# Kernel tuning notes

Measured on AMD Instinct MI355X. Metric: run time of the kernel, lower is better.

The kernel has to match this reference:

```python
import jax, jax.numpy as jnp
import numpy as np

N = 100000
E = 1600000
IN_DIM, H1, H2, C = 256, 128, 128, 32


def setup_inputs() -> dict:
    key = jax.random.key(0)
    ks = jax.random.split(key, 8)
    X = jax.random.normal(ks[0], (N, IN_DIM), dtype=jnp.float32)
    edge_index = jax.random.randint(ks[1], (2, E), 0, N, dtype=jnp.int64)
    def glorot(k, shape):
        fan_in, fan_out = shape[0], shape[1]
        lim = (6.0 / (fan_in + fan_out)) ** 0.5
        return jax.random.uniform(k, shape, jnp.float32, -lim, lim)
    W1 = glorot(ks[2], (IN_DIM, H1))
    b1 = jnp.zeros((H1,), jnp.float32)
    W2 = glorot(ks[3], (H1, H2))
    b2 = jnp.zeros((H2,), jnp.float32)
    Wc = glorot(ks[4], (H2, C))
    bc = jnp.zeros((C,), jnp.float32)
    return {"X": X, "edge_index": edge_index, "W1": W1, "b1": b1,
            "W2": W2, "b2": b2, "Wc": Wc, "bc": bc}


def gcn_conv(x, src, dst, dinv, W, b, n):
    # PyG GCNConv: transform, then sym-normalized scatter-add with self-loops
    x = x @ W  # [N, out]
    norm = dinv[src] * dinv[dst]  # [E+N]
    msgs = x[src] * norm[:, None]  # [E+N, out] gather along edges
    out = jax.ops.segment_sum(msgs, dst, num_segments=n)
    return out + b


def reference(X, edge_index, W1, b1, W2, b2, Wc, bc):
    n = X.shape[0]
    loop = jnp.arange(n, dtype=edge_index.dtype)
    src = jnp.concatenate([edge_index[0], loop])
    dst = jnp.concatenate([edge_index[1], loop])
    # degree (with self-loops) at destination nodes
    deg = jax.ops.segment_sum(jnp.ones_like(dst, jnp.float32), dst, num_segments=n)
    dinv = jnp.where(deg > 0, jax.lax.rsqrt(deg), 0.0)
    h = jax.nn.relu(gcn_conv(X, src, dst, dinv, W1, b1, n))
    h = jax.nn.relu(gcn_conv(h, src, dst, dinv, W2, b2, n))
    logits = h @ Wc + bc
    return logits
```

## Files before the change

kernel.cpp:

```cpp
#include <hip/hip_runtime.h>
#include <hip/hip_bf16.h>
#include <hip/hip_fp16.h>

#define IN_DIM 256
#define HDIM 128
#define CDIM 32
#define NSUB 512
#define PCHUNK 4096

typedef __attribute__((ext_vector_type(8))) unsigned short u16x8;
typedef __attribute__((ext_vector_type(8))) _Float16 f16x8;
typedef __attribute__((ext_vector_type(4))) float f32x4;
typedef __attribute__((ext_vector_type(4))) int int4v;

__device__ __forceinline__ int swz4(int r) { return (r & 3) ^ ((r >> 2) & 3); }


__global__ void zero512_kernel(int* __restrict__ p) {
    p[blockIdx.x * 256 + threadIdx.x] = 0;
}

__global__ __launch_bounds__(256) void hist512_kernel(const int* __restrict__ dst,
                                                      int* __restrict__ cnt512, int e, int nsr) {
    __shared__ int h[NSUB];
    for (int j = threadIdx.x; j < NSUB; j += 256) h[j] = 0;
    __syncthreads();
    const int stride = gridDim.x * 256;
    for (int i = blockIdx.x * 256 + threadIdx.x; i < e; i += stride) {
        int d = __builtin_nontemporal_load(&dst[i]);
        atomicAdd(&h[(unsigned)d / (unsigned)nsr], 1);
    }
    __syncthreads();
    for (int j = threadIdx.x; j < NSUB; j += 256)
        if (h[j]) atomicAdd(&cnt512[j], h[j]);
}

__global__ __launch_bounds__(256) void scan512_kernel(const int* __restrict__ cnt512,
                                                      int* __restrict__ rp512,
                                                      int* __restrict__ rcur512, int e) {
    __shared__ int sd[256];
    int t = threadIdx.x;
    int v0 = cnt512[2 * t], v1 = cnt512[2 * t + 1];
    sd[t] = v0 + v1;
    __syncthreads();
    for (int off = 1; off < 256; off <<= 1) {
        int x = (t >= off) ? sd[t - off] : 0;
        __syncthreads();
        sd[t] += x;
        __syncthreads();
    }
    int excl = sd[t] - (v0 + v1);
    rp512[2 * t] = excl;          rcur512[2 * t] = excl;
    rp512[2 * t + 1] = excl + v0; rcur512[2 * t + 1] = excl + v0;
    if (t == 255) rp512[512] = e;
}

__global__ __launch_bounds__(256) void part512_kernel(
        const int* __restrict__ src, const int* __restrict__ dst,
        int* __restrict__ rcur512, long long* __restrict__ parts, int e, int nsr) {
    __shared__ long long staged[PCHUNK];
    __shared__ int hist[NSUB], lbase[NSUB], gbase[NSUB], lcur[NSUB];
    __shared__ int sd[256];
    const int t = threadIdx.x;
    const int nch = (e + PCHUNK - 1) / PCHUNK;
    for (int c = blockIdx.x; c < nch; c += gridDim.x) {
        const int b0 = c * PCHUNK;
        const int cnt = (b0 + PCHUNK <= e) ? PCHUNK : (e - b0);
        int s[16], d[16], bn[16];
        hist[2 * t] = 0; hist[2 * t + 1] = 0;
        __syncthreads();
        if (cnt == PCHUNK) {
#pragma unroll
            for (int q = 0; q < 4; ++q) {
                int u = q * 256 + t;
                int4v sv = __builtin_nontemporal_load((const int4v*)(src + b0) + u);
                int4v dv = __builtin_nontemporal_load((const int4v*)(dst + b0) + u);
                s[4 * q] = sv.x; s[4 * q + 1] = sv.y; s[4 * q + 2] = sv.z; s[4 * q + 3] = sv.w;
                d[4 * q] = dv.x; d[4 * q + 1] = dv.y; d[4 * q + 2] = dv.z; d[4 * q + 3] = dv.w;
            }
#pragma unroll
            for (int j = 0; j < 16; ++j) {
                bn[j] = (int)((unsigned)d[j] / (unsigned)nsr);
                atomicAdd(&hist[bn[j]], 1);
            }
        } else {
#pragma unroll
            for (int j = 0; j < 16; ++j) {
                int u = (j / 4) * 1024 + t * 4 + (j & 3);
                int i = b0 + u;
                if (u < cnt) {
                    s[j] = src[i]; d[j] = dst[i];
                    bn[j] = (int)((unsigned)d[j] / (unsigned)nsr);
                    atomicAdd(&hist[bn[j]], 1);
                } else bn[j] = -1;
            }
        }
        __syncthreads();
        int h0 = hist[2 * t], h1 = hist[2 * t + 1];
        sd[t] = h0 + h1;
        __syncthreads();
        for (int off = 1; off < 256; off <<= 1) {
            int x = (t >= off) ? sd[t - off] : 0;
            __syncthreads();
            sd[t] += x;
            __syncthreads();
        }
        int excl = sd[t] - (h0 + h1);
        lbase[2 * t] = excl;          lcur[2 * t] = excl;
        lbase[2 * t + 1] = excl + h0; lcur[2 * t + 1] = excl + h0;
        gbase[2 * t]     = h0 ? atomicAdd(&rcur512[2 * t], h0) : 0;
        gbase[2 * t + 1] = h1 ? atomicAdd(&rcur512[2 * t + 1], h1) : 0;
        __syncthreads();
#pragma unroll
        for (int j = 0; j < 16; ++j) {
            if (bn[j] >= 0) {
                int pos = atomicAdd(&lcur[bn[j]], 1);
                staged[pos] = ((long long)(unsigned)d[j] << 32) | (unsigned)s[j];
            }
        }
        __syncthreads();
        for (int i = t; i < cnt; i += 256) {
            long long v = staged[i];
            int b = (int)((unsigned)(int)(v >> 32) / (unsigned)nsr);
            parts[gbase[b] + (i - lbase[b])] = v;
        }
        __syncthreads();
    }
}

__global__ __launch_bounds__(256) void sortplace_kernel(
        const long long* __restrict__ parts, const int* __restrict__ rp512,
        int* __restrict__ row_ptr, int* __restrict__ csr_src, float* __restrict__ dinv,
        int n, int nsr) {
    __shared__ int hist[256], sd[256], cur[256];
    const int b = blockIdx.x;
    const int d0 = b * nsr;
    if (d0 > n) return;
    const int i0 = rp512[b], iE = rp512[b + 1];
    const int t = threadIdx.x;
    hist[t] = 0;
    __syncthreads();
    for (int i = i0 + t; i < iE; i += 256) {
        int d = (int)(parts[i] >> 32);
        atomicAdd(&hist[d - d0], 1);
    }
    __syncthreads();
    int v = hist[t];
    sd[t] = v;
    __syncthreads();
    for (int off = 1; off < 256; off <<= 1) {
        int x = (t >= off) ? sd[t - off] : 0;
        __syncthreads();
        sd[t] += x;
        __syncthreads();
    }
    int excl = sd[t] - v;
    int node = d0 + t;
    if (t <= nsr && node <= n) row_ptr[node] = i0 + excl;
    if (t < nsr && node < n) dinv[node] = rsqrtf((float)(v + 1));
    cur[t] = i0 + excl;
    __syncthreads();
    for (int i = i0 + t; i < iE; i += 256) {
        long long vv = parts[i];
        int d = (int)(vv >> 32);
        int pos = atomicAdd(&cur[d - d0], 1);
        csr_src[pos] = (int)(vv & 0xffffffffLL);
    }
}


__global__ void wconv_all_kernel(const float* __restrict__ W1, const float* __restrict__ W2,
                                 const float* __restrict__ Wc,
                                 unsigned short* __restrict__ w1t, unsigned short* __restrict__ w2t,
                                 unsigned short* __restrict__ wct) {
    int i = blockIdx.x * 256 + threadIdx.x;
    const int s1 = IN_DIM * HDIM;
    const int s2 = s1 + HDIM * HDIM;
    const int s3 = s2 + HDIM * CDIM;
    if (i < s1) {
        int k = i / HDIM, n2 = i % HDIM;
        w1t[n2 * IN_DIM + k] = __half_as_ushort(__float2half_rn(W1[i]));
    } else if (i < s2) {
        int j = i - s1; int k = j / HDIM, n2 = j % HDIM;
        w2t[n2 * HDIM + k] = __half_as_ushort(__float2half_rn(W2[j]));
    } else if (i < s3) {
        int j = i - s2; int k = j / CDIM, n2 = j % CDIM;
        wct[n2 * HDIM + k] = __half_as_ushort(__float2half_rn(Wc[j]));
    }
}


template<int BN, bool AF16, bool BIAS, bool OUTH>
__global__ __launch_bounds__(256) void gemm_f16_kernel(
        const void* __restrict__ Ap, const unsigned short* __restrict__ Wt,
        const float* __restrict__ bias, void* __restrict__ C, int M, int K) {
    constexpr int FM = 4;
    constexpr int FN = BN / 2 / 16;
    constexpr int BU = (BN * 4 + 255) / 256;
    __shared__ __align__(16) unsigned short As[2][128 * 32];
    __shared__ __align__(16) unsigned short Bs[2][BN * 32];

    const int t = threadIdx.x;
    const int rowBase = blockIdx.x * 128;
    const int l = t & 63, w = t >> 6;
    const int wr = w >> 1, wc = w & 1;
    const int lrow = l & 15, g = l >> 4;
    const int NK = K >> 5;

    f32x4 acc[FM][FN];
#pragma unroll
    for (int i = 0; i < FM; ++i)
#pragma unroll
        for (int j = 0; j < FN; ++j) acc[i][j] = f32x4{0.f, 0.f, 0.f, 0.f};

    u16x8 aS[2];
    float4 af[2][2];
    u16x8 bS[BU];

    auto LOADA = [&](int k0) {
#pragma unroll
        for (int i = 0; i < 2; ++i) {
            int u = t + 256 * i;
            int r = u >> 2, c = u & 3;
            int gr = rowBase + r; if (gr > M - 1) gr = M - 1;
            if (AF16) {
                aS[i] = ((const u16x8*)((const unsigned short*)Ap + (size_t)gr * K + k0))[c];
            } else {
                const float4* ar = (const float4*)((const float*)Ap + (size_t)gr * K + k0);
                af[i][0] = ar[c * 2];
                af[i][1] = ar[c * 2 + 1];
            }
        }
    };
    auto WRITEA = [&](int buf) {
#pragma unroll
        for (int i = 0; i < 2; ++i) {
            int u = t + 256 * i;
            int r = u >> 2, c = u & 3;
            int d = r * 4 + (c ^ swz4(r));
            if (AF16) {
                ((u16x8*)As[buf])[d] = aS[i];
            } else {
                f16x8 h;
                h[0] = (_Float16)af[i][0].x; h[1] = (_Float16)af[i][0].y;
                h[2] = (_Float16)af[i][0].z; h[3] = (_Float16)af[i][0].w;
                h[4] = (_Float16)af[i][1].x; h[5] = (_Float16)af[i][1].y;
                h[6] = (_Float16)af[i][1].z; h[7] = (_Float16)af[i][1].w;
                ((f16x8*)As[buf])[d] = h;
            }
        }
    };
    auto LOADB = [&](int k0) {
#pragma unroll
        for (int i = 0; i < BU; ++i) {
            int u = t + 256 * i;
            if (u < BN * 4) {
                int nn = u >> 2, c = u & 3;
                bS[i] = ((const u16x8*)(Wt + (size_t)nn * K + k0))[c];
            }
        }
    };
    auto WRITEB = [&](int buf) {
#pragma unroll
        for (int i = 0; i < BU; ++i) {
            int u = t + 256 * i;
            if (u < BN * 4) {
                int nn = u >> 2, c = u & 3;
                ((u16x8*)Bs[buf])[nn * 4 + (c ^ swz4(nn))] = bS[i];
            }
        }
    };

    LOADA(0); LOADB(0);
    WRITEA(0); WRITEB(0);
    __syncthreads();

    for (int k = 0; k < NK; ++k) {
        int cur = k & 1;
        bool more = (k + 1 < NK);
        if (more) { LOADA((k + 1) << 5); LOADB((k + 1) << 5); }

        f16x8 a[FM], b[FN];
#pragma unroll
        for (int fm = 0; fm < FM; ++fm) {
            int r = wr * 64 + fm * 16 + lrow;
            a[fm] = ((const f16x8*)As[cur])[r * 4 + (g ^ swz4(r))];
        }
#pragma unroll
        for (int fn = 0; fn < FN; ++fn) {
            int nn = wc * (FN * 16) + fn * 16 + lrow;
            b[fn] = ((const f16x8*)Bs[cur])[nn * 4 + (g ^ swz4(nn))];
        }
#pragma unroll
        for (int fm = 0; fm < FM; ++fm)
#pragma unroll
            for (int fn = 0; fn < FN; ++fn)
                acc[fm][fn] = __builtin_amdgcn_mfma_f32_16x16x32_f16(a[fm], b[fn], acc[fm][fn], 0, 0, 0);

        if (more) { WRITEA(cur ^ 1); WRITEB(cur ^ 1); }
        __syncthreads();
    }

#pragma unroll
    for (int fm = 0; fm < FM; ++fm)
#pragma unroll
        for (int fn = 0; fn < FN; ++fn) {
            int col = wc * (FN * 16) + fn * 16 + lrow;
#pragma unroll
            for (int r = 0; r < 4; ++r) {
                int row = rowBase + wr * 64 + fm * 16 + g * 4 + r;
                if (row < M) {
                    float v = acc[fm][fn][r];
                    if (BIAS) v += bias[col];
                    if (OUTH) {
                        __builtin_nontemporal_store(
                            __half_as_ushort(__float2half_rn(v)),
                            (unsigned short*)C + (size_t)row * BN + col);
                    } else {
                        ((float*)C)[(size_t)row * BN + col] = v;
                    }
                }
            }
        }
}


__global__ __launch_bounds__(256) void gather_kernel(
        const __half* __restrict__ x, const int* __restrict__ row_ptr,
        const int* __restrict__ csr_src, const float* __restrict__ dinv,
        const float* __restrict__ bias, __half* __restrict__ out, int n) {
    int node = __builtin_amdgcn_readfirstlane(blockIdx.x * 4 + (threadIdx.x >> 6));
    if (node >= n) return;
    int lane = threadIdx.x & 63;
    const __half2* xv = (const __half2*)x;
    float dd = dinv[node];
    float2 self = __half22float2(xv[(size_t)node * 64 + lane]);
    float accx = dd * self.x, accy = dd * self.y;
    int p = row_ptr[node], end = row_ptr[node + 1];
    for (; p + 7 < end; p += 8) {
        int s[8]; float w[8]; float2 v[8];
#pragma unroll
        for (int j = 0; j < 8; ++j) s[j] = csr_src[p + j];
#pragma unroll
        for (int j = 0; j < 8; ++j) w[j] = dinv[s[j]];
#pragma unroll
        for (int j = 0; j < 8; ++j) v[j] = __half22float2(xv[(size_t)s[j] * 64 + lane]);
#pragma unroll
        for (int j = 0; j < 8; ++j) { accx += w[j] * v[j].x; accy += w[j] * v[j].y; }
    }
    for (; p + 3 < end; p += 4) {
        int s0 = csr_src[p], s1 = csr_src[p + 1], s2 = csr_src[p + 2], s3 = csr_src[p + 3];
        float w0 = dinv[s0], w1 = dinv[s1], w2 = dinv[s2], w3 = dinv[s3];
        float2 v0 = __half22float2(xv[(size_t)s0 * 64 + lane]);
        float2 v1 = __half22float2(xv[(size_t)s1 * 64 + lane]);
        float2 v2 = __half22float2(xv[(size_t)s2 * 64 + lane]);
        float2 v3 = __half22float2(xv[(size_t)s3 * 64 + lane]);
        accx += w0 * v0.x + w1 * v1.x + w2 * v2.x + w3 * v3.x;
        accy += w0 * v0.y + w1 * v1.y + w2 * v2.y + w3 * v3.y;
    }
    for (; p < end; ++p) {
        int s0 = csr_src[p];
        float w0 = dinv[s0];
        float2 v0 = __half22float2(xv[(size_t)s0 * 64 + lane]);
        accx += w0 * v0.x;
        accy += w0 * v0.y;
    }
    float2 bb = ((const float2*)bias)[lane];
    float2 r;
    r.x = fmaxf(accx * dd + bb.x, 0.f);
    r.y = fmaxf(accy * dd + bb.y, 0.f);
    __half2 hv = __float22half2_rn(r);
    __builtin_nontemporal_store(*(unsigned int*)&hv,
                                (unsigned int*)((__half2*)out + (size_t)node * 64 + lane));
}


__global__ __launch_bounds__(256) void gather_cls_kernel(
        const __half* __restrict__ x, const int* __restrict__ row_ptr,
        const int* __restrict__ csr_src, const float* __restrict__ dinv,
        const float* __restrict__ b2, const unsigned short* __restrict__ wct,
        const float* __restrict__ bc, float* __restrict__ out, int n) {
    __shared__ __align__(16) __half h_lds[16][136];
    const int w = threadIdx.x >> 6;
    const int lane = threadIdx.x & 63;
    const int node0 = blockIdx.x * 16;
    const __half2* xv = (const __half2*)x;
    const float2 bb = ((const float2*)b2)[lane];

#pragma unroll
    for (int j = 0; j < 4; ++j) {
        int row = w * 4 + j;
        int node = __builtin_amdgcn_readfirstlane(node0 + row);
        float2 rv = make_float2(0.f, 0.f);
        if (node < n) {
            float dd = dinv[node];
            float2 self = __half22float2(xv[(size_t)node * 64 + lane]);
            float accx = dd * self.x, accy = dd * self.y;
            int p = row_ptr[node], end = row_ptr[node + 1];
            for (; p + 7 < end; p += 8) {
                int s[8]; float wt[8]; float2 v[8];
#pragma unroll
                for (int q = 0; q < 8; ++q) s[q] = csr_src[p + q];
#pragma unroll
                for (int q = 0; q < 8; ++q) wt[q] = dinv[s[q]];
#pragma unroll
                for (int q = 0; q < 8; ++q) v[q] = __half22float2(xv[(size_t)s[q] * 64 + lane]);
#pragma unroll
                for (int q = 0; q < 8; ++q) { accx += wt[q] * v[q].x; accy += wt[q] * v[q].y; }
            }
            for (; p + 3 < end; p += 4) {
                int s0 = csr_src[p], s1 = csr_src[p + 1], s2 = csr_src[p + 2], s3 = csr_src[p + 3];
                float w0 = dinv[s0], w1 = dinv[s1], w2 = dinv[s2], w3 = dinv[s3];
                float2 v0 = __half22float2(xv[(size_t)s0 * 64 + lane]);
                float2 v1 = __half22float2(xv[(size_t)s1 * 64 + lane]);
                float2 v2 = __half22float2(xv[(size_t)s2 * 64 + lane]);
                float2 v3 = __half22float2(xv[(size_t)s3 * 64 + lane]);
                accx += w0 * v0.x + w1 * v1.x + w2 * v2.x + w3 * v3.x;
                accy += w0 * v0.y + w1 * v1.y + w2 * v2.y + w3 * v3.y;
            }
            for (; p < end; ++p) {
                int s0 = csr_src[p];
                float w0 = dinv[s0];
                float2 v0 = __half22float2(xv[(size_t)s0 * 64 + lane]);
                accx += w0 * v0.x;
                accy += w0 * v0.y;
            }
            rv.x = fmaxf(accx * dd + bb.x, 0.f);
            rv.y = fmaxf(accy * dd + bb.y, 0.f);
        }
        *(__half2*)&h_lds[row][2 * lane] = __float22half2_rn(rv);
    }
    __syncthreads();

    if (w == 0) {
        const int lrow = lane & 15, g = lane >> 4;
        f32x4 acc[2];
        acc[0] = f32x4{0.f, 0.f, 0.f, 0.f};
        acc[1] = f32x4{0.f, 0.f, 0.f, 0.f};
#pragma unroll
        for (int k0 = 0; k0 < HDIM; k0 += 32) {
            f16x8 a = *(const f16x8*)&h_lds[lrow][k0 + 8 * g];
#pragma unroll
            for (int fn = 0; fn < 2; ++fn) {
                f16x8 b = *(const f16x8*)((const _Float16*)wct + (fn * 16 + lrow) * HDIM + k0 + 8 * g);
                acc[fn] = __builtin_amdgcn_mfma_f32_16x16x32_f16(a, b, acc[fn], 0, 0, 0);
            }
        }
#pragma unroll
        for (int fn = 0; fn < 2; ++fn) {
            int col = fn * 16 + lrow;
            float bcv = bc[col];
#pragma unroll
            for (int r = 0; r < 4; ++r) {
                int node = node0 + g * 4 + r;
                if (node < n) out[(size_t)node * CDIM + col] = acc[fn][r] + bcv;
            }
        }
    }
}


extern "C" void kernel_launch(void* const* d_in, const int* in_sizes, int n_in,
                              void* d_out, int out_size, void* d_ws, size_t ws_size,
                              hipStream_t stream) {
    const float* X  = (const float*)d_in[0];
    const int*   ei = (const int*)d_in[1];
    const float* W1 = (const float*)d_in[2];
    const float* b1 = (const float*)d_in[3];
    const float* W2 = (const float*)d_in[4];
    const float* b2 = (const float*)d_in[5];
    const float* Wc = (const float*)d_in[6];
    const float* bc = (const float*)d_in[7];
    float* out = (float*)d_out;

    const int n = in_sizes[0] / IN_DIM;
    const int e = in_sizes[1] / 2;
    const int* src = ei;
    const int* dst = ei + e;
    const int nsr = (n + NSUB - 1) / NSUB;

    char* ws = (char*)d_ws;
    auto align = [](size_t x) { return (x + 255) & ~(size_t)255; };
    size_t off = 0;
    float* dinv   = (float*)(ws + off); off += align((size_t)n * 4);
    int* row_ptr  = (int*)(ws + off);   off += align((size_t)(n + 1) * 4);
    int* cnt512   = (int*)(ws + off);   off += align(512 * 4);
    int* rp512    = (int*)(ws + off);   off += align(513 * 4);
    int* rcur512  = (int*)(ws + off);   off += align(512 * 4);
    long long* parts = (long long*)(ws + off); off += align((size_t)e * 8);
    int* csr_src  = (int*)(ws + off);   off += align((size_t)e * 4);
    unsigned short* w1t = (unsigned short*)(ws + off); off += align((size_t)IN_DIM * HDIM * 2);
    unsigned short* w2t = (unsigned short*)(ws + off); off += align((size_t)HDIM * HDIM * 2);
    unsigned short* wct = (unsigned short*)(ws + off); off += align((size_t)HDIM * CDIM * 2);
    __half* bufAh = (__half*)(ws + off); off += align((size_t)n * HDIM * 2);
    __half* bufBh = (__half*)(ws + off); off += align((size_t)n * HDIM * 2);

    wconv_all_kernel<<<(IN_DIM * HDIM + HDIM * HDIM + HDIM * CDIM + 255) / 256, 256, 0, stream>>>(
        W1, W2, Wc, w1t, w2t, wct);

    zero512_kernel<<<2, 256, 0, stream>>>(cnt512);
    hist512_kernel<<<256, 256, 0, stream>>>(dst, cnt512, e, nsr);
    scan512_kernel<<<1, 256, 0, stream>>>(cnt512, rp512, rcur512, e);
    part512_kernel<<<512, 256, 0, stream>>>(src, dst, rcur512, parts, e, nsr);
    sortplace_kernel<<<NSUB, 256, 0, stream>>>(parts, rp512, row_ptr, csr_src, dinv, n, nsr);

    const int gBlocks = (n + 127) / 128;
    const int nb_g = (n + 3) / 4;

    gemm_f16_kernel<128, false, false, true><<<gBlocks, 256, 0, stream>>>(X, w1t, nullptr, bufAh, n, IN_DIM);
    gather_kernel<<<nb_g, 256, 0, stream>>>(bufAh, row_ptr, csr_src, dinv, b1, bufBh, n);

    gemm_f16_kernel<128, true, false, true><<<gBlocks, 256, 0, stream>>>(bufBh, w2t, nullptr, bufAh, n, HDIM);

    gather_cls_kernel<<<(n + 15) / 16, 256, 0, stream>>>(bufAh, row_ptr, csr_src, dinv, b2, wct, bc, out, n);
}
```

Baseline: 249.2 us.

## Store hidden features in column-blocked layout and gather per 16-column slice

The GEMM outputs are now written in a column-blocked fp16 layout, with 16 columns per block stored contiguously across all nodes. The gather kernel is rewritten so each block handles one 16-column slice for 32 nodes, using 8 lanes per node. The aim is to keep each slice's gathered working set (~3.2MB) cache-resident and improve reuse of the random neighbor reads. The fused gather+classifier kernel is split into a second gather plus a separate classifier GEMM with bias, which adds one extra kernel and one extra round trip of the hidden features. Each slice also re-reads csr_src and dinv, eight times in total, using nontemporal loads for the indices.

```diff
diff --git a/kernel.cpp b/kernel.cpp
--- a/kernel.cpp
+++ b/kernel.cpp
@@ -190,7 +190,7 @@
 }
 
 
-template<int BN, bool AF16, bool BIAS, bool OUTH>
+template<int BN, int AMODE, bool BIAS, int OMODE>
 __global__ __launch_bounds__(256) void gemm_f16_kernel(
         const void* __restrict__ Ap, const unsigned short* __restrict__ Wt,
         const float* __restrict__ bias, void* __restrict__ C, int M, int K) {
@@ -223,8 +223,9 @@
             int u = t + 256 * i;
             int r = u >> 2, c = u & 3;
             int gr = rowBase + r; if (gr > M - 1) gr = M - 1;
-            if (AF16) {
-                aS[i] = ((const u16x8*)((const unsigned short*)Ap + (size_t)gr * K + k0))[c];
+            if (AMODE == 1) {
+                int colbase = k0 + c * 8;
+                aS[i] = ((const u16x8*)Ap)[((size_t)(colbase >> 4) * M + gr) * 2 + ((colbase >> 3) & 1)];
             } else {
                 const float4* ar = (const float4*)((const float*)Ap + (size_t)gr * K + k0);
                 af[i][0] = ar[c * 2];
@@ -238,7 +239,7 @@
             int u = t + 256 * i;
             int r = u >> 2, c = u & 3;
             int d = r * 4 + (c ^ swz4(r));
-            if (AF16) {
+            if (AMODE == 1) {
                 ((u16x8*)As[buf])[d] = aS[i];
             } else {
                 f16x8 h;
@@ -312,10 +313,10 @@
                 if (row < M) {
                     float v = acc[fm][fn][r];
                     if (BIAS) v += bias[col];
-                    if (OUTH) {
+                    if (OMODE == 1) {
                         __builtin_nontemporal_store(
                             __half_as_ushort(__float2half_rn(v)),
-                            (unsigned short*)C + (size_t)row * BN + col);
+                            (unsigned short*)C + ((size_t)(col >> 4) * M + row) * 16 + (col & 15));
                     } else {
                         ((float*)C)[(size_t)row * BN + col] = v;
                     }
@@ -325,138 +326,48 @@
 }
 
 
-__global__ __launch_bounds__(256) void gather_kernel(
-        const __half* __restrict__ x, const int* __restrict__ row_ptr,
+__global__ __launch_bounds__(256) void gather_cb_kernel(
+        const __half* __restrict__ xcb, const int* __restrict__ row_ptr,
         const int* __restrict__ csr_src, const float* __restrict__ dinv,
-        const float* __restrict__ bias, __half* __restrict__ out, int n) {
-    int node = __builtin_amdgcn_readfirstlane(blockIdx.x * 4 + (threadIdx.x >> 6));
+        const float* __restrict__ bias, __half* __restrict__ outcb, int n) {
+    const int g = blockIdx.x & 7;
+    const int chunk = blockIdx.x >> 3;
+    const int t = threadIdx.x;
+    const int sub = t >> 3, cl = t & 7;
+    const int node = chunk * 32 + sub;
     if (node >= n) return;
-    int lane = threadIdx.x & 63;
-    const __half2* xv = (const __half2*)x;
+    const __half2* xs = (const __half2*)xcb + (size_t)g * n * 8;
+    const float2 bb = ((const float2*)bias)[g * 8 + cl];
     float dd = dinv[node];
-    float2 self = __half22float2(xv[(size_t)node * 64 + lane]);
-    float accx = dd * self.x, accy = dd * self.y;
+    float2 self = __half22float2(xs[(size_t)node * 8 + cl]);
+    float ax = dd * self.x, ay = dd * self.y;
     int p = row_ptr[node], end = row_ptr[node + 1];
-    for (; p + 7 < end; p += 8) {
-        int s[8]; float w[8]; float2 v[8];
-#pragma unroll
-        for (int j = 0; j < 8; ++j) s[j] = csr_src[p + j];
-#pragma unroll
-        for (int j = 0; j < 8; ++j) w[j] = dinv[s[j]];
-#pragma unroll
-        for (int j = 0; j < 8; ++j) v[j] = __half22float2(xv[(size_t)s[j] * 64 + lane]);
-#pragma unroll
-        for (int j = 0; j < 8; ++j) { accx += w[j] * v[j].x; accy += w[j] * v[j].y; }
-    }
     for (; p + 3 < end; p += 4) {
-        int s0 = csr_src[p], s1 = csr_src[p + 1], s2 = csr_src[p + 2], s3 = csr_src[p + 3];
+        int s0 = __builtin_nontemporal_load(&csr_src[p]);
+        int s1 = __builtin_nontemporal_load(&csr_src[p + 1]);
+        int s2 = __builtin_nontemporal_load(&csr_src[p + 2]);
+        int s3 = __builtin_nontemporal_load(&csr_src[p + 3]);
         float w0 = dinv[s0], w1 = dinv[s1], w2 = dinv[s2], w3 = dinv[s3];
-        float2 v0 = __half22float2(xv[(size_t)s0 * 64 + lane]);
-        float2 v1 = __half22float2(xv[(size_t)s1 * 64 + lane]);
-        float2 v2 = __half22float2(xv[(size_t)s2 * 64 + lane]);
-        float2 v3 = __half22float2(xv[(size_t)s3 * 64 + lane]);
-        accx += w0 * v0.x + w1 * v1.x + w2 * v2.x + w3 * v3.x;
-        accy += w0 * v0.y + w1 * v1.y + w2 * v2.y + w3 * v3.y;
+        float2 v0 = __half22float2(xs[(size_t)s0 * 8 + cl]);
+        float2 v1 = __half22float2(xs[(size_t)s1 * 8 + cl]);
+        float2 v2 = __half22float2(xs[(size_t)s2 * 8 + cl]);
+        float2 v3 = __half22float2(xs[(size_t)s3 * 8 + cl]);
+        ax += w0 * v0.x + w1 * v1.x + w2 * v2.x + w3 * v3.x;
+        ay += w0 * v0.y + w1 * v1.y + w2 * v2.y + w3 * v3.y;
     }
     for (; p < end; ++p) {
         int s0 = csr_src[p];
         float w0 = dinv[s0];
-        float2 v0 = __half22float2(xv[(size_t)s0 * 64 + lane]);
-        accx += w0 * v0.x;
-        accy += w0 * v0.y;
-    }
-    float2 bb = ((const float2*)bias)[lane];
+        float2 v0 = __half22float2(xs[(size_t)s0 * 8 + cl]);
+        ax += w0 * v0.x;
+        ay += w0 * v0.y;
+    }
     float2 r;
-    r.x = fmaxf(accx * dd + bb.x, 0.f);
-    r.y = fmaxf(accy * dd + bb.y, 0.f);
+    r.x = fmaxf(ax * dd + bb.x, 0.f);
+    r.y = fmaxf(ay * dd + bb.y, 0.f);
     __half2 hv = __float22half2_rn(r);
     __builtin_nontemporal_store(*(unsigned int*)&hv,
-                                (unsigned int*)((__half2*)out + (size_t)node * 64 + lane));
-}
-
-
-__global__ __launch_bounds__(256) void gather_cls_kernel(
-        const __half* __restrict__ x, const int* __restrict__ row_ptr,
-        const int* __restrict__ csr_src, const float* __restrict__ dinv,
-        const float* __restrict__ b2, const unsigned short* __restrict__ wct,
-        const float* __restrict__ bc, float* __restrict__ out, int n) {
-    __shared__ __align__(16) __half h_lds[16][136];
-    const int w = threadIdx.x >> 6;
-    const int lane = threadIdx.x & 63;
-    const int node0 = blockIdx.x * 16;
-    const __half2* xv = (const __half2*)x;
-    const float2 bb = ((const float2*)b2)[lane];
-
-#pragma unroll
-    for (int j = 0; j < 4; ++j) {
-        int row = w * 4 + j;
-        int node = __builtin_amdgcn_readfirstlane(node0 + row);
-        float2 rv = make_float2(0.f, 0.f);
-        if (node < n) {
-            float dd = dinv[node];
-            float2 self = __half22float2(xv[(size_t)node * 64 + lane]);
-            float accx = dd * self.x, accy = dd * self.y;
-            int p = row_ptr[node], end = row_ptr[node + 1];
-            for (; p + 7 < end; p += 8) {
-                int s[8]; float wt[8]; float2 v[8];
-#pragma unroll
-                for (int q = 0; q < 8; ++q) s[q] = csr_src[p + q];
-#pragma unroll
-                for (int q = 0; q < 8; ++q) wt[q] = dinv[s[q]];
-#pragma unroll
-                for (int q = 0; q < 8; ++q) v[q] = __half22float2(xv[(size_t)s[q] * 64 + lane]);
-#pragma unroll
-                for (int q = 0; q < 8; ++q) { accx += wt[q] * v[q].x; accy += wt[q] * v[q].y; }
-            }
-            for (; p + 3 < end; p += 4) {
-                int s0 = csr_src[p], s1 = csr_src[p + 1], s2 = csr_src[p + 2], s3 = csr_src[p + 3];
-                float w0 = dinv[s0], w1 = dinv[s1], w2 = dinv[s2], w3 = dinv[s3];
-                float2 v0 = __half22float2(xv[(size_t)s0 * 64 + lane]);
-                float2 v1 = __half22float2(xv[(size_t)s1 * 64 + lane]);
-                float2 v2 = __half22float2(xv[(size_t)s2 * 64 + lane]);
-                float2 v3 = __half22float2(xv[(size_t)s3 * 64 + lane]);
-                accx += w0 * v0.x + w1 * v1.x + w2 * v2.x + w3 * v3.x;
-                accy += w0 * v0.y + w1 * v1.y + w2 * v2.y + w3 * v3.y;
-            }
-            for (; p < end; ++p) {
-                int s0 = csr_src[p];
-                float w0 = dinv[s0];
-                float2 v0 = __half22float2(xv[(size_t)s0 * 64 + lane]);
-                accx += w0 * v0.x;
-                accy += w0 * v0.y;
-            }
-            rv.x = fmaxf(accx * dd + bb.x, 0.f);
-            rv.y = fmaxf(accy * dd + bb.y, 0.f);
-        }
-        *(__half2*)&h_lds[row][2 * lane] = __float22half2_rn(rv);
-    }
-    __syncthreads();
-
-    if (w == 0) {
-        const int lrow = lane & 15, g = lane >> 4;
-        f32x4 acc[2];
-        acc[0] = f32x4{0.f, 0.f, 0.f, 0.f};
-        acc[1] = f32x4{0.f, 0.f, 0.f, 0.f};
-#pragma unroll
-        for (int k0 = 0; k0 < HDIM; k0 += 32) {
-            f16x8 a = *(const f16x8*)&h_lds[lrow][k0 + 8 * g];
-#pragma unroll
-            for (int fn = 0; fn < 2; ++fn) {
-                f16x8 b = *(const f16x8*)((const _Float16*)wct + (fn * 16 + lrow) * HDIM + k0 + 8 * g);
-                acc[fn] = __builtin_amdgcn_mfma_f32_16x16x32_f16(a, b, acc[fn], 0, 0, 0);
-            }
-        }
-#pragma unroll
-        for (int fn = 0; fn < 2; ++fn) {
-            int col = fn * 16 + lrow;
-            float bcv = bc[col];
-#pragma unroll
-            for (int r = 0; r < 4; ++r) {
-                int node = node0 + g * 4 + r;
-                if (node < n) out[(size_t)node * CDIM + col] = acc[fn][r] + bcv;
-            }
-        }
-    }
+        (unsigned int*)((__half2*)outcb + (size_t)g * n * 8 + (size_t)node * 8 + cl));
 }
 
 
@@ -505,12 +416,13 @@
     sortplace_kernel<<<NSUB, 256, 0, stream>>>(parts, rp512, row_ptr, csr_src, dinv, n, nsr);
 
     const int gBlocks = (n + 127) / 128;
-    const int nb_g = (n + 3) / 4;
-
-    gemm_f16_kernel<128, false, false, true><<<gBlocks, 256, 0, stream>>>(X, w1t, nullptr, bufAh, n, IN_DIM);
-    gather_kernel<<<nb_g, 256, 0, stream>>>(bufAh, row_ptr, csr_src, dinv, b1, bufBh, n);
-
-    gemm_f16_kernel<128, true, false, true><<<gBlocks, 256, 0, stream>>>(bufBh, w2t, nullptr, bufAh, n, HDIM);
-
-    gather_cls_kernel<<<(n + 15) / 16, 256, 0, stream>>>(bufAh, row_ptr, csr_src, dinv, b2, wct, bc, out, n);
-}
+    const int gaBlocks = ((n + 31) / 32) * 8;
+
+    gemm_f16_kernel<128, 0, false, 1><<<gBlocks, 256, 0, stream>>>(X, w1t, nullptr, bufAh, n, IN_DIM);
+    gather_cb_kernel<<<gaBlocks, 256, 0, stream>>>(bufAh, row_ptr, csr_src, dinv, b1, bufBh, n);
+
+    gemm_f16_kernel<128, 1, false, 1><<<gBlocks, 256, 0, stream>>>(bufBh, w2t, nullptr, bufAh, n, HDIM);
+    gather_cb_kernel<<<gaBlocks, 256, 0, stream>>>(bufAh, row_ptr, csr_src, dinv, b2, bufBh, n);
+
+    gemm_f16_kernel<32, 1, true, 0><<<gBlocks, 256, 0, stream>>>(bufBh, wct, bc, out, n, HDIM);
+}
```

Measured after the change: 536.9 us. 115% more time.
